# Kernel tuning notes

Hardware: AMD Instinct MI355X
Metric: run time of the kernel (lower is better)

The kernel has to match this reference:

```python
import jax, jax.numpy as jnp
import numpy as np

NEG_POS_RATIO = 3
THETA = 0.01
NUM_CLASSES = 21
B, P = 64, 16320
POS_FRAC = 0.02


def setup_inputs() -> dict:
    key = jax.random.key(0)
    k1, k2, k3, k4, k5, k6 = jax.random.split(key, 6)
    loc_data = jax.random.normal(k1, (B, P, 4), dtype=jnp.float32)
    conf_data = jax.random.normal(k2, (B, P, NUM_CLASSES), dtype=jnp.float32)
    arm_conf_data = jax.random.normal(k3, (B, P, 2), dtype=jnp.float32)
    loc_t = jax.random.normal(k4, (B, P, 4), dtype=jnp.float32)
    labels = jax.random.randint(k5, (B, P), 1, NUM_CLASSES)
    is_pos = jax.random.uniform(k6, (B, P)) < POS_FRAC
    conf_t = jnp.where(is_pos, labels, 0).astype(jnp.int64)
    return {"loc_data": loc_data, "conf_data": conf_data,
            "arm_conf_data": arm_conf_data, "loc_t": loc_t, "conf_t": conf_t}


def _multibox_loss(loc_data, conf_data, arm_conf_data, loc_t, conf_t):
    num_priors = conf_t.shape[1]
    # ODM: zero out positives whose ARM objectness score P(obj) <= theta
    p_obj = jax.nn.softmax(arm_conf_data, axis=-1)[:, :, 1]          # [B,P]
    pos = (conf_t > 0) & (p_obj > THETA)                             # [B,P]

    # localization loss: smooth L1 over positive anchors (masked sum == masked gather + sum)
    diff = loc_data - loc_t
    ad = jnp.abs(diff)
    sl1 = jnp.where(ad < 1.0, 0.5 * ad * ad, ad - 0.5)               # [B,P,4]
    loss_l = jnp.sum(sl1 * pos[..., None].astype(sl1.dtype))

    # per-anchor CE loss: logsumexp(c) - c[target]
    lse = jax.nn.logsumexp(conf_data, axis=-1)                       # [B,P]
    true_logit = jnp.take_along_axis(conf_data, conf_t[..., None], axis=-1)[..., 0]
    loss_c_all = lse - true_logit                                    # [B,P]

    # hard negative mining: rank non-positive anchors by loss (double argsort)
    loss_for_rank = jnp.where(pos, 0.0, loss_c_all)
    rank = jnp.argsort(jnp.argsort(-loss_for_rank, axis=1), axis=1)  # [B,P]
    num_pos = jnp.sum(pos.astype(jnp.int32), axis=1, keepdims=True)  # [B,1]
    num_neg = jnp.minimum(NEG_POS_RATIO * num_pos, num_priors - 1)
    neg = rank < num_neg                                             # [B,P]

    sel = pos | neg
    loss_c = jnp.sum(jnp.where(sel, loss_c_all, 0.0))

    N = jnp.sum(num_pos).astype(loss_l.dtype)
    return loss_l / N, loss_c / N


def reference(loc_data, conf_data, arm_conf_data, loc_t, conf_t):
    return _multibox_loss(loc_data, conf_data, arm_conf_data, loc_t, conf_t)
```

## Files before the change

kernel.cpp:

```cpp
#include <hip/hip_runtime.h>

#define NUM_P 16320
#define NUM_C 21
#define THETA 0.01f
#define WAVES_PER_ROW (NUM_P / 64)

__global__ __launch_bounds__(256) void anchor_kernel(
    const float* __restrict__ loc, const float* __restrict__ conf,
    const float* __restrict__ arm, const float* __restrict__ loct,
    const int* __restrict__ conft,
    int* __restrict__ partial_n, float* __restrict__ rankvals,
    float* __restrict__ partial_l, float* __restrict__ partial_c,
    int ntiles)
{
    __shared__ float tile[256 * NUM_C];
    __shared__ float red_l[4], red_c[4];
    const int tid = threadIdx.x;
    const int lane = tid & 63, w = tid >> 6;
    const int stride = gridDim.x;

    int t = blockIdx.x;
    if (t >= ntiles) return;

    float4 rr[6];
    int    tc_n;
    float2 av_n;

    {
        const int base = t * 256;
        const float4* conf4 = (const float4*)(conf + (size_t)base * NUM_C);
        #pragma unroll
        for (int it = 0; it < 6; ++it) {
            const int i = tid + it * 256;
            if (i < 1344) rr[it] = conf4[i];
        }
        tc_n = conft[base + tid];
        av_n = ((const float2*)arm)[base + tid];
    }

    while (true) {
        const int a = t * 256 + tid;
        const int    tc = tc_n;
        const float2 av = av_n;

        {
            float4* tile4 = (float4*)tile;
            #pragma unroll
            for (int it = 0; it < 6; ++it) {
                const int i = tid + it * 256;
                if (i < 1344) tile4[i] = rr[it];
            }
        }
        __syncthreads();

        const int tn = t + stride;
        if (tn < ntiles) {
            const int nbase = tn * 256;
            const float4* conf4 = (const float4*)(conf + (size_t)nbase * NUM_C);
            #pragma unroll
            for (int it = 0; it < 6; ++it) {
                const int i = tid + it * 256;
                if (i < 1344) rr[it] = conf4[i];
            }
            tc_n = conft[nbase + tid];
            av_n = ((const float2*)arm)[nbase + tid];
        }

        float ll = 0.f, cep = 0.f;
        bool pos = false;
        {
            const float* cf = &tile[tid * NUM_C];
            float mx = cf[0];
            #pragma unroll
            for (int j = 1; j < NUM_C; ++j) mx = fmaxf(mx, cf[j]);
            float s = 0.f;
            #pragma unroll
            for (int j = 0; j < NUM_C; ++j) s += __expf(cf[j] - mx);
            const float ce = mx + __logf(s) - cf[tc];

            const float am = fmaxf(av.x, av.y);
            const float e0 = __expf(av.x - am), e1 = __expf(av.y - am);
            const float p1 = e1 / (e0 + e1);
            pos = (tc > 0) && (p1 > THETA);

            if (pos) {
                cep = ce;
                const float4 lv = ((const float4*)loc)[a];
                const float4 tv = ((const float4*)loct)[a];
                const float dx[4] = { lv.x - tv.x, lv.y - tv.y, lv.z - tv.z, lv.w - tv.w };
                #pragma unroll
                for (int j = 0; j < 4; ++j) {
                    const float ad = fabsf(dx[j]);
                    ll += (ad < 1.f) ? 0.5f * ad * ad : ad - 0.5f;
                }
            }
            rankvals[a] = pos ? 0.f : ce;
        }

        const unsigned long long pm = __ballot(pos);
        #pragma unroll
        for (int off = 32; off > 0; off >>= 1) {
            ll  += __shfl_down(ll, off, 64);
            cep += __shfl_down(cep, off, 64);
        }
        if (lane == 0) {
            red_l[w] = ll;
            red_c[w] = cep;
            partial_n[t * 4 + w] = (int)__popcll(pm);
        }
        __syncthreads();
        if (tid == 0) {
            partial_l[t] = red_l[0] + red_l[1] + red_l[2] + red_l[3];
            partial_c[t] = red_c[0] + red_c[1] + red_c[2] + red_c[3];
        }
        if (tn >= ntiles) break;
        t = tn;
        __syncthreads();
    }
}

__global__ __launch_bounds__(1024) void select_kernel(
    const float* __restrict__ rankvals, const int* __restrict__ partial_n,
    const float* __restrict__ partial_l, const float* __restrict__ partial_c,
    float* __restrict__ acc,
    int ntiles, float* __restrict__ out)
{
    __shared__ int hist[256];
    __shared__ unsigned s_prefix;
    __shared__ int s_kk;
    __shared__ int s_np;
    __shared__ float wsum[16], wsl[16], wsc[16];

    const int b = blockIdx.x;
    const int tid = threadIdx.x;
    const int lane = tid & 63, w = tid >> 6;

    const uint4* row4 = (const uint4*)(rankvals + (size_t)b * NUM_P);
    uint4 rr[4];
    #pragma unroll
    for (int it = 0; it < 4; ++it) {
        const int i = tid + it * 1024;
        rr[it] = (i < NUM_P / 4) ? row4[i] : make_uint4(0u, 0u, 0u, 0u);
    }
    int rn = (tid < WAVES_PER_ROW) ? partial_n[b * WAVES_PER_ROW + tid] : 0;

    float sl = 0.f, sc = 0.f;
    {
        const int slice = (ntiles + gridDim.x - 1) / gridDim.x;
        const int s0 = b * slice;
        const int s1 = min(s0 + slice, ntiles);
        for (int i = s0 + tid; i < s1; i += 1024) { sl += partial_l[i]; sc += partial_c[i]; }
    }

    if (tid == 0) s_np = 0;
    if (tid < 256) hist[tid] = 0;
    __syncthreads();

    #pragma unroll
    for (int off = 32; off > 0; off >>= 1) {
        rn += __shfl_down(rn, off, 64);
        sl += __shfl_down(sl, off, 64);
        sc += __shfl_down(sc, off, 64);
    }
    if (lane == 0) {
        wsl[w] = sl; wsc[w] = sc;
        if (rn) atomicAdd(&s_np, rn);
    }
    __syncthreads();

    const int np = s_np;
    const int k = min(3 * np, NUM_P - 1);

    float tot = 0.f;
    int kk = 0;
    float vth = 0.f;

    if (k > 0) {
        unsigned prefix = 0, himask = 0;
        kk = k;

        for (int pass = 0; pass < 4; ++pass) {
            const int shift = 24 - 8 * pass;

            if (pass == 0) {
                #pragma unroll
                for (int it = 0; it < 4; ++it) {
                    const unsigned ub[4] = { rr[it].x, rr[it].y, rr[it].z, rr[it].w };
                    #pragma unroll
                    for (int j = 0; j < 4; ++j) {
                        const unsigned bin = ub[j] >> 24;
                        unsigned long long alive = ~0ULL;
                        while (alive) {
                            const int leader = __ffsll(alive) - 1;
                            const unsigned lb = __shfl(bin, leader, 64);
                            const unsigned long long mm = __ballot(bin == lb);
                            if (lane == leader) atomicAdd(&hist[lb], (int)__popcll(mm));
                            alive &= ~mm;
                        }
                    }
                }
            } else {
                #pragma unroll
                for (int it = 0; it < 4; ++it) {
                    const unsigned ub[4] = { rr[it].x, rr[it].y, rr[it].z, rr[it].w };
                    #pragma unroll
                    for (int j = 0; j < 4; ++j) {
                        const unsigned u = ub[j];
                        if ((u & himask) == prefix)
                            atomicAdd(&hist[(u >> shift) & 255u], 1);
                    }
                }
            }
            __syncthreads();

            if (tid < 64) {
                const int j0 = tid * 4;
                const int h0 = hist[j0], h1 = hist[j0 + 1], h2 = hist[j0 + 2], h3 = hist[j0 + 3];
                int ssum = h0 + h1 + h2 + h3;
                #pragma unroll
                for (int d = 1; d < 64; d <<= 1) {
                    const int tmp = __shfl_down(ssum, d, 64);
                    if (lane + d < 64) ssum += tmp;
                }
                const int bse = ssum - (h0 + h1 + h2 + h3);
                int S[5];
                S[0] = ssum; S[4] = bse;
                S[3] = bse + h3; S[2] = S[3] + h2; S[1] = S[2] + h1;
                #pragma unroll
                for (int jj = 0; jj < 4; ++jj) {
                    if (S[jj] >= kk && S[jj + 1] < kk) {
                        s_prefix = prefix | ((unsigned)(j0 + jj) << shift);
                        s_kk = kk - S[jj + 1];
                    }
                }
            }
            __syncthreads();
            prefix = s_prefix;
            kk = s_kk;
            himask |= (0xFFu << shift);
            if (tid < 256) hist[tid] = 0;
            __syncthreads();
        }

        const unsigned vbits = prefix;
        vth = __uint_as_float(vbits);

        float partial = 0.f;
        #pragma unroll
        for (int it = 0; it < 4; ++it) {
            const unsigned ub[4] = { rr[it].x, rr[it].y, rr[it].z, rr[it].w };
            #pragma unroll
            for (int j = 0; j < 4; ++j)
                if (ub[j] > vbits) partial += __uint_as_float(ub[j]);
        }
        #pragma unroll
        for (int off = 32; off > 0; off >>= 1)
            partial += __shfl_down(partial, off, 64);
        if (lane == 0) wsum[w] = partial;
        __syncthreads();
        if (tid == 0) {
            #pragma unroll
            for (int wv = 0; wv < 16; ++wv) tot += wsum[wv];
            tot += (float)kk * vth;
        }
    }

    if (tid == 0) {
        float SL = 0.f, SC = 0.f;
        #pragma unroll
        for (int wv = 0; wv < 16; ++wv) { SL += wsl[wv]; SC += wsc[wv]; }
        int* acc_i = (int*)acc;
        atomicAdd(&acc[0], SL);
        atomicAdd(&acc[1], SC + tot);
        atomicAdd(&acc_i[2], np);
        __threadfence();
        const int prev = atomicAdd(&acc_i[3], 1);
        if (prev == (int)gridDim.x - 1) {
            __threadfence();
            const float L = atomicAdd(&acc[0], 0.f);
            const float C = atomicAdd(&acc[1], 0.f);
            const int   N = atomicAdd(&acc_i[2], 0);
            out[0] = L / (float)N;
            out[1] = C / (float)N;
        }
    }
}

extern "C" void kernel_launch(void* const* d_in, const int* in_sizes, int n_in,
                              void* d_out, int out_size, void* d_ws, size_t ws_size,
                              hipStream_t stream) {
    const float* loc  = (const float*)d_in[0];
    const float* conf = (const float*)d_in[1];
    const float* arm  = (const float*)d_in[2];
    const float* loct = (const float*)d_in[3];
    const int*  conft = (const int*)d_in[4];
    float* out = (float*)d_out;

    const int total  = in_sizes[4];
    const int Bn     = total / NUM_P;
    const int ntiles = total / 256;

    float* acc       = (float*)d_ws;
    float* partial_l = (float*)((char*)d_ws + 1024);
    float* partial_c = (float*)((char*)d_ws + 17408);
    int*   partial_n = (int*)((char*)d_ws + 33792);
    float* rankvals  = (float*)((char*)d_ws + 99328);

    hipMemsetAsync(d_ws, 0, 64, stream);

    const int grid = min(ntiles, 7 * 256);
    hipLaunchKernelGGL(anchor_kernel, dim3(grid), dim3(256), 0, stream,
                       loc, conf, arm, loct, conft, partial_n, rankvals,
                       partial_l, partial_c, ntiles);
    hipLaunchKernelGGL(select_kernel, dim3(Bn), dim3(1024), 0, stream,
                       rankvals, partial_n, partial_l, partial_c, acc, ntiles, out);
}
```

Baseline: 201.6 us.

## Double-buffer conf prefetch two tiles ahead and shorten top-k radix select

```diff
diff --git a/kernel.cpp b/kernel.cpp
--- a/kernel.cpp
+++ b/kernel.cpp
@@ -3,9 +3,104 @@
 #define NUM_P 16320
 #define NUM_C 21
 #define THETA 0.01f
-#define WAVES_PER_ROW (NUM_P / 64)
-
-__global__ __launch_bounds__(256) void anchor_kernel(
+#define WPR 255
+
+__device__ __forceinline__ void load_tile(
+    const float* __restrict__ conf, const int* __restrict__ conft,
+    const float* __restrict__ arm, int t, int tid,
+    float4 (&rr)[6], int& tc, float2& av)
+{
+    const int base = t * 256;
+    const float4* conf4 = (const float4*)(conf + (size_t)base * NUM_C);
+    #pragma unroll
+    for (int it = 0; it < 6; ++it) {
+        const int i = tid + it * 256;
+        if (i < 1344) rr[it] = conf4[i];
+    }
+    tc = conft[base + tid];
+    av = ((const float2*)arm)[base + tid];
+}
+
+__device__ __forceinline__ void process_tile(
+    const float* __restrict__ loc, const float* __restrict__ loct,
+    const float* __restrict__ conf, const int* __restrict__ conft,
+    const float* __restrict__ arm,
+    int* __restrict__ partial_n, float* __restrict__ rankvals,
+    float* __restrict__ partial_l, float* __restrict__ partial_c,
+    int t, int stride, int ntiles, int tid,
+    float* tile, float* red_l, float* red_c,
+    float4 (&rr)[6], int& tc, float2& av)
+{
+    const int lane = tid & 63, w = tid >> 6;
+    const int tcl = tc;
+    const float2 avl = av;
+
+    __syncthreads();
+    {
+        float4* tile4 = (float4*)tile;
+        #pragma unroll
+        for (int it = 0; it < 6; ++it) {
+            const int i = tid + it * 256;
+            if (i < 1344) tile4[i] = rr[it];
+        }
+    }
+    __syncthreads();
+
+    const int tpre = t + 2 * stride;
+    if (tpre < ntiles)
+        load_tile(conf, conft, arm, tpre, tid, rr, tc, av);
+
+    const int a = t * 256 + tid;
+    float ll = 0.f, cep = 0.f;
+    bool pos = false;
+    {
+        const float* cf = &tile[tid * NUM_C];
+        float mx = cf[0];
+        #pragma unroll
+        for (int j = 1; j < NUM_C; ++j) mx = fmaxf(mx, cf[j]);
+        float s = 0.f;
+        #pragma unroll
+        for (int j = 0; j < NUM_C; ++j) s += __expf(cf[j] - mx);
+        const float ce = mx + __logf(s) - cf[tcl];
+
+        const float am = fmaxf(avl.x, avl.y);
+        const float e0 = __expf(avl.x - am), e1 = __expf(avl.y - am);
+        const float p1 = e1 / (e0 + e1);
+        pos = (tcl > 0) && (p1 > THETA);
+
+        if (pos) {
+            cep = ce;
+            const float4 lv = ((const float4*)loc)[a];
+            const float4 tv = ((const float4*)loct)[a];
+            const float dx[4] = { lv.x - tv.x, lv.y - tv.y, lv.z - tv.z, lv.w - tv.w };
+            #pragma unroll
+            for (int j = 0; j < 4; ++j) {
+                const float ad = fabsf(dx[j]);
+                ll += (ad < 1.f) ? 0.5f * ad * ad : ad - 0.5f;
+            }
+        }
+        rankvals[a] = pos ? 0.f : ce;
+    }
+
+    const unsigned long long pm = __ballot(pos);
+    #pragma unroll
+    for (int off = 32; off > 0; off >>= 1) {
+        ll  += __shfl_down(ll, off, 64);
+        cep += __shfl_down(cep, off, 64);
+    }
+    if (lane == 0) {
+        red_l[w] = ll;
+        red_c[w] = cep;
+        partial_n[t * 4 + w] = (int)__popcll(pm);
+    }
+    __syncthreads();
+    if (tid == 0) {
+        partial_l[t] = red_l[0] + red_l[1] + red_l[2] + red_l[3];
+        partial_c[t] = red_c[0] + red_c[1] + red_c[2] + red_c[3];
+    }
+}
+
+__global__ __launch_bounds__(256, 4) void anchor_kernel(
     const float* __restrict__ loc, const float* __restrict__ conf,
     const float* __restrict__ arm, const float* __restrict__ loct,
     const int* __restrict__ conft,
@@ -16,106 +111,28 @@
     __shared__ float tile[256 * NUM_C];
     __shared__ float red_l[4], red_c[4];
     const int tid = threadIdx.x;
-    const int lane = tid & 63, w = tid >> 6;
     const int stride = gridDim.x;
 
     int t = blockIdx.x;
     if (t >= ntiles) return;
 
-    float4 rr[6];
-    int    tc_n;
-    float2 av_n;
-
-    {
-        const int base = t * 256;
-        const float4* conf4 = (const float4*)(conf + (size_t)base * NUM_C);
-        #pragma unroll
-        for (int it = 0; it < 6; ++it) {
-            const int i = tid + it * 256;
-            if (i < 1344) rr[it] = conf4[i];
-        }
-        tc_n = conft[base + tid];
-        av_n = ((const float2*)arm)[base + tid];
-    }
+    float4 rA[6]; int tcA; float2 avA;
+    float4 rB[6]; int tcB; float2 avB;
+    load_tile(conf, conft, arm, t, tid, rA, tcA, avA);
+    if (t + stride < ntiles)
+        load_tile(conf, conft, arm, t + stride, tid, rB, tcB, avB);
 
     while (true) {
-        const int a = t * 256 + tid;
-        const int    tc = tc_n;
-        const float2 av = av_n;
-
-        {
-            float4* tile4 = (float4*)tile;
-            #pragma unroll
-            for (int it = 0; it < 6; ++it) {
-                const int i = tid + it * 256;
-                if (i < 1344) tile4[i] = rr[it];
-            }
-        }
-        __syncthreads();
-
-        const int tn = t + stride;
-        if (tn < ntiles) {
-            const int nbase = tn * 256;
-            const float4* conf4 = (const float4*)(conf + (size_t)nbase * NUM_C);
-            #pragma unroll
-            for (int it = 0; it < 6; ++it) {
-                const int i = tid + it * 256;
-                if (i < 1344) rr[it] = conf4[i];
-            }
-            tc_n = conft[nbase + tid];
-            av_n = ((const float2*)arm)[nbase + tid];
-        }
-
-        float ll = 0.f, cep = 0.f;
-        bool pos = false;
-        {
-            const float* cf = &tile[tid * NUM_C];
-            float mx = cf[0];
-            #pragma unroll
-            for (int j = 1; j < NUM_C; ++j) mx = fmaxf(mx, cf[j]);
-            float s = 0.f;
-            #pragma unroll
-            for (int j = 0; j < NUM_C; ++j) s += __expf(cf[j] - mx);
-            const float ce = mx + __logf(s) - cf[tc];
-
-            const float am = fmaxf(av.x, av.y);
-            const float e0 = __expf(av.x - am), e1 = __expf(av.y - am);
-            const float p1 = e1 / (e0 + e1);
-            pos = (tc > 0) && (p1 > THETA);
-
-            if (pos) {
-                cep = ce;
-                const float4 lv = ((const float4*)loc)[a];
-                const float4 tv = ((const float4*)loct)[a];
-                const float dx[4] = { lv.x - tv.x, lv.y - tv.y, lv.z - tv.z, lv.w - tv.w };
-                #pragma unroll
-                for (int j = 0; j < 4; ++j) {
-                    const float ad = fabsf(dx[j]);
-                    ll += (ad < 1.f) ? 0.5f * ad * ad : ad - 0.5f;
-                }
-            }
-            rankvals[a] = pos ? 0.f : ce;
-        }
-
-        const unsigned long long pm = __ballot(pos);
-        #pragma unroll
-        for (int off = 32; off > 0; off >>= 1) {
-            ll  += __shfl_down(ll, off, 64);
-            cep += __shfl_down(cep, off, 64);
-        }
-        if (lane == 0) {
-            red_l[w] = ll;
-            red_c[w] = cep;
-            partial_n[t * 4 + w] = (int)__popcll(pm);
-        }
-        __syncthreads();
-        if (tid == 0) {
-            partial_l[t] = red_l[0] + red_l[1] + red_l[2] + red_l[3];
-            partial_c[t] = red_c[0] + red_c[1] + red_c[2] + red_c[3];
-        }
-        if (tn >= ntiles) break;
-        t = tn;
-        __syncthreads();
+        process_tile(loc, loct, conf, conft, arm, partial_n, rankvals,
+                     partial_l, partial_c, t, stride, ntiles, tid,
+                     tile, red_l, red_c, rA, tcA, avA);
+        t += stride;
+        if (t >= ntiles) break;
+        process_tile(loc, loct, conf, conft, arm, partial_n, rankvals,
+                     partial_l, partial_c, t, stride, ntiles, tid,
+                     tile, red_l, red_c, rB, tcB, avB);
+        t += stride;
+        if (t >= ntiles) break;
     }
 }
 
@@ -125,14 +142,12 @@
     float* __restrict__ acc,
     int ntiles, float* __restrict__ out)
 {
-    __shared__ int hist[256];
-    __shared__ unsigned s_prefix;
-    __shared__ int s_kk;
-    __shared__ int s_np;
-    __shared__ float wsum[16], wsl[16], wsc[16];
-
-    const int b = blockIdx.x;
-    const int tid = threadIdx.x;
+    __shared__ int hist1[256];
+    __shared__ int hist2[2048];
+    __shared__ float wred[16], wsl[16], wsc[16];
+    __shared__ int s_b1, s_kk1, s_t19, s_kk2, s_np;
+
+    const int b = blockIdx.x, tid = threadIdx.x;
     const int lane = tid & 63, w = tid >> 6;
 
     const uint4* row4 = (const uint4*)(rankvals + (size_t)b * NUM_P);
@@ -142,18 +157,18 @@
         const int i = tid + it * 1024;
         rr[it] = (i < NUM_P / 4) ? row4[i] : make_uint4(0u, 0u, 0u, 0u);
     }
-    int rn = (tid < WAVES_PER_ROW) ? partial_n[b * WAVES_PER_ROW + tid] : 0;
+    int rn = (tid < WPR) ? partial_n[b * WPR + tid] : 0;
 
     float sl = 0.f, sc = 0.f;
     {
         const int slice = (ntiles + gridDim.x - 1) / gridDim.x;
-        const int s0 = b * slice;
-        const int s1 = min(s0 + slice, ntiles);
+        const int s0 = b * slice, s1 = min(s0 + slice, ntiles);
         for (int i = s0 + tid; i < s1; i += 1024) { sl += partial_l[i]; sc += partial_c[i]; }
     }
 
     if (tid == 0) s_np = 0;
-    if (tid < 256) hist[tid] = 0;
+    if (tid < 256) hist1[tid] = 0;
+    hist2[tid] = 0; hist2[tid + 1024] = 0;
     __syncthreads();
 
     #pragma unroll
@@ -170,98 +185,93 @@
 
     const int np = s_np;
     const int k = min(3 * np, NUM_P - 1);
-
     float tot = 0.f;
-    int kk = 0;
-    float vth = 0.f;
 
     if (k > 0) {
-        unsigned prefix = 0, himask = 0;
-        kk = k;
-
-        for (int pass = 0; pass < 4; ++pass) {
-            const int shift = 24 - 8 * pass;
-
-            if (pass == 0) {
-                #pragma unroll
-                for (int it = 0; it < 4; ++it) {
-                    const unsigned ub[4] = { rr[it].x, rr[it].y, rr[it].z, rr[it].w };
-                    #pragma unroll
-                    for (int j = 0; j < 4; ++j) {
-                        const unsigned bin = ub[j] >> 24;
-                        unsigned long long alive = ~0ULL;
-                        while (alive) {
-                            const int leader = __ffsll(alive) - 1;
-                            const unsigned lb = __shfl(bin, leader, 64);
-                            const unsigned long long mm = __ballot(bin == lb);
-                            if (lane == leader) atomicAdd(&hist[lb], (int)__popcll(mm));
-                            alive &= ~mm;
-                        }
-                    }
-                }
-            } else {
-                #pragma unroll
-                for (int it = 0; it < 4; ++it) {
-                    const unsigned ub[4] = { rr[it].x, rr[it].y, rr[it].z, rr[it].w };
-                    #pragma unroll
-                    for (int j = 0; j < 4; ++j) {
-                        const unsigned u = ub[j];
-                        if ((u & himask) == prefix)
-                            atomicAdd(&hist[(u >> shift) & 255u], 1);
-                    }
+        #pragma unroll
+        for (int it = 0; it < 4; ++it) {
+            const unsigned ub[4] = { rr[it].x, rr[it].y, rr[it].z, rr[it].w };
+            #pragma unroll
+            for (int j = 0; j < 4; ++j) {
+                const unsigned bin = ub[j] >> 24;
+                unsigned long long alive = ~0ULL;
+                while (alive) {
+                    const int leader = __ffsll(alive) - 1;
+                    const unsigned lb = __shfl(bin, leader, 64);
+                    const unsigned long long mm = __ballot(bin == lb);
+                    if (lane == leader) atomicAdd(&hist1[lb], (int)__popcll(mm));
+                    alive &= ~mm;
                 }
             }
-            __syncthreads();
-
-            if (tid < 64) {
-                const int j0 = tid * 4;
-                const int h0 = hist[j0], h1 = hist[j0 + 1], h2 = hist[j0 + 2], h3 = hist[j0 + 3];
-                int ssum = h0 + h1 + h2 + h3;
-                #pragma unroll
-                for (int d = 1; d < 64; d <<= 1) {
-                    const int tmp = __shfl_down(ssum, d, 64);
-                    if (lane + d < 64) ssum += tmp;
-                }
-                const int bse = ssum - (h0 + h1 + h2 + h3);
-                int S[5];
-                S[0] = ssum; S[4] = bse;
-                S[3] = bse + h3; S[2] = S[3] + h2; S[1] = S[2] + h1;
-                #pragma unroll
-                for (int jj = 0; jj < 4; ++jj) {
-                    if (S[jj] >= kk && S[jj + 1] < kk) {
-                        s_prefix = prefix | ((unsigned)(j0 + jj) << shift);
-                        s_kk = kk - S[jj + 1];
-                    }
-                }
+        }
+        __syncthreads();
+        if (tid < 64) {
+            const int j0 = tid * 4;
+            const int h0 = hist1[j0], h1 = hist1[j0+1], h2 = hist1[j0+2], h3 = hist1[j0+3];
+            int ssum = h0 + h1 + h2 + h3;
+            #pragma unroll
+            for (int d = 1; d < 64; d <<= 1) {
+                const int tmp = __shfl_down(ssum, d, 64);
+                if (lane + d < 64) ssum += tmp;
             }
-            __syncthreads();
-            prefix = s_prefix;
-            kk = s_kk;
-            himask |= (0xFFu << shift);
-            if (tid < 256) hist[tid] = 0;
-            __syncthreads();
-        }
-
-        const unsigned vbits = prefix;
-        vth = __uint_as_float(vbits);
-
-        float partial = 0.f;
+            const int bse = ssum - (h0 + h1 + h2 + h3);
+            int S[5];
+            S[0] = ssum; S[4] = bse;
+            S[3] = bse + h3; S[2] = S[3] + h2; S[1] = S[2] + h1;
+            #pragma unroll
+            for (int jj = 0; jj < 4; ++jj)
+                if (S[jj] >= k && S[jj + 1] < k) { s_b1 = j0 + jj; s_kk1 = k - S[jj + 1]; }
+        }
+        __syncthreads();
+        const unsigned B1 = (unsigned)s_b1;
+        const int kk1 = s_kk1;
+
         #pragma unroll
         for (int it = 0; it < 4; ++it) {
             const unsigned ub[4] = { rr[it].x, rr[it].y, rr[it].z, rr[it].w };
             #pragma unroll
             for (int j = 0; j < 4; ++j)
-                if (ub[j] > vbits) partial += __uint_as_float(ub[j]);
+                if ((ub[j] >> 24) == B1) atomicAdd(&hist2[(ub[j] >> 13) & 0x7FFu], 1);
+        }
+        __syncthreads();
+        const int h0 = hist2[2 * tid], h1 = hist2[2 * tid + 1];
+        int suf = h0 + h1;
+        #pragma unroll
+        for (int d = 1; d < 64; d <<= 1) {
+            const int tmp = __shfl_down(suf, d, 64);
+            if (lane + d < 64) suf += tmp;
+        }
+        if (lane == 0) hist1[w] = suf;
+        __syncthreads();
+        int woff = 0;
+        for (int ww = w + 1; ww < 16; ++ww) woff += hist1[ww];
+        const int S0 = suf + woff;
+        const int S1 = S0 - h0;
+        const int S2 = S1 - h1;
+        if (S0 >= kk1 && S1 < kk1) { s_t19 = (s_b1 << 11) | (2 * tid);     s_kk2 = kk1 - S1; }
+        if (S1 >= kk1 && S2 < kk1) { s_t19 = (s_b1 << 11) | (2 * tid + 1); s_kk2 = kk1 - S2; }
+        __syncthreads();
+        const unsigned t19 = (unsigned)s_t19;
+        const int kk2 = s_kk2;
+        const float vth = __uint_as_float(t19 << 13);
+
+        float partial = 0.f;
+        #pragma unroll
+        for (int it = 0; it < 4; ++it) {
+            const unsigned ub[4] = { rr[it].x, rr[it].y, rr[it].z, rr[it].w };
+            #pragma unroll
+            for (int j = 0; j < 4; ++j)
+                if ((ub[j] >> 13) > t19) partial += __uint_as_float(ub[j]);
         }
         #pragma unroll
         for (int off = 32; off > 0; off >>= 1)
             partial += __shfl_down(partial, off, 64);
-        if (lane == 0) wsum[w] = partial;
+        if (lane == 0) wred[w] = partial;
         __syncthreads();
         if (tid == 0) {
             #pragma unroll
-            for (int wv = 0; wv < 16; ++wv) tot += wsum[wv];
-            tot += (float)kk * vth;
+            for (int wv = 0; wv < 16; ++wv) tot += wred[wv];
+            tot += (float)kk2 * vth;
         }
     }
 
@@ -308,7 +318,7 @@
 
     hipMemsetAsync(d_ws, 0, 64, stream);
 
-    const int grid = min(ntiles, 7 * 256);
+    const int grid = min(ntiles, 1024);
     hipLaunchKernelGGL(anchor_kernel, dim3(grid), dim3(256), 0, stream,
                        loc, conf, arm, loct, conft, partial_n, rankvals,
                        partial_l, partial_c, ntiles);
```

After: 205.8 us. +2.1%, slower.
